# Optimization experiments

Hardware: AMD Instinct MI355X
Metric: run time of the kernel (lower is better)

Reference implementation:

```python
import jax, jax.numpy as jnp
import numpy as np

C, K, DIL = 128, 3, 1
PAD = DIL
KK = K * K
EPS = 1e-5


def setup_inputs() -> dict:
    key = jax.random.key(0)
    k0, k1, k2 = jax.random.split(key, 3)
    B, H, W = 8, 128, 128
    x = jax.random.normal(k0, (B, C, H, W), jnp.float32)
    # small offset-conv weights so predicted offsets are realistic (sub-pixel scale)
    w_off = jax.random.normal(k1, (2 * KK, C, K, K), jnp.float32) * 0.01
    b_off = jnp.zeros((2 * KK,), jnp.float32)
    w_dw = jax.random.normal(k2, (C, 1, K, K), jnp.float32) * (1.0 / 3.0)
    gamma = jnp.ones((C,), jnp.float32)
    beta = jnp.zeros((C,), jnp.float32)
    return {"x": x, "w_off": w_off, "b_off": b_off, "w_dw": w_dw,
            "gamma": gamma, "beta": beta}


def _deform_depthwise(x, offset, w_dw):
    """torchvision-style deform_conv2d, groups=C (depthwise), stride=1."""
    B, C_, H, W = x.shape
    off = offset.reshape(B, KK, 2, H, W)  # (y,x) pairs per kernel tap
    hs = jnp.arange(H, dtype=x.dtype)[None, None, :, None]
    ws = jnp.arange(W, dtype=x.dtype)[None, None, None, :]
    ki = jnp.arange(K, dtype=x.dtype)
    ky = jnp.repeat(ki, K)  # [KK] row index of tap
    kx = jnp.tile(ki, K)    # [KK] col index of tap
    # sampling positions: base grid + dilated tap offset - pad + learned offset
    py = hs + (DIL * ky - PAD)[None, :, None, None] + off[:, :, 0]  # [B,KK,H,W]
    px = ws + (DIL * kx - PAD)[None, :, None, None] + off[:, :, 1]
    y0 = jnp.floor(py)
    x0 = jnp.floor(px)
    ty = py - y0
    tx = px - x0
    y0i = y0.astype(jnp.int32)
    x0i = x0.astype(jnp.int32)

    def gather(xb, yi, xi):
        # zero outside the image (torchvision zero-pad semantics)
        valid = (yi >= 0) & (yi < H) & (xi >= 0) & (xi < W)
        yc = jnp.clip(yi, 0, H - 1)
        xc = jnp.clip(xi, 0, W - 1)
        v = xb[:, yc, xc]  # [C,KK,H,W]
        return v * valid[None].astype(xb.dtype)

    def sample_one(xb, y0b, x0b, tyb, txb):
        v00 = gather(xb, y0b, x0b)
        v01 = gather(xb, y0b, x0b + 1)
        v10 = gather(xb, y0b + 1, x0b)
        v11 = gather(xb, y0b + 1, x0b + 1)
        w00 = (1 - tyb) * (1 - txb)
        w01 = (1 - tyb) * txb
        w10 = tyb * (1 - txb)
        w11 = tyb * txb
        return (v00 * w00[None] + v01 * w01[None]
                + v10 * w10[None] + v11 * w11[None])  # [C,KK,H,W]

    val = jax.vmap(sample_one)(x, y0i, x0i, ty, tx)  # [B,C,KK,H,W]
    # depthwise contraction over the KK taps
    return jnp.einsum('bckhw,ck->bchw', val, w_dw.reshape(C, KK))


def reference(x, w_off, b_off, w_dw, gamma, beta):
    identity = x
    offset = jax.lax.conv_general_dilated(
        x, w_off, window_strides=(1, 1), padding=[(PAD, PAD), (PAD, PAD)],
        dimension_numbers=('NCHW', 'OIHW', 'NCHW'))
    offset = offset + b_off[None, :, None, None]
    out = _deform_depthwise(x, offset, w_dw)
    # BatchNorm2d in training mode (batch statistics), then SiLU
    mean = jnp.mean(out, axis=(0, 2, 3), keepdims=True)
    var = jnp.mean((out - mean) ** 2, axis=(0, 2, 3), keepdims=True)
    out = (out - mean) * jax.lax.rsqrt(var + EPS)
    out = out * gamma[None, :, None, None] + beta[None, :, None, None]
    out = out * jax.nn.sigmoid(out)  # SiLU
    return out + identity
```

## Files before the change

kernel.cpp:

```cpp
#include <hip/hip_runtime.h>
#include <hip/hip_fp16.h>
#include <math.h>

#define Cc 128
#define Hh 128
#define Ww 128
#define Bb 8
#define HW 16384
#define NPIX 131072
#define NOFF 18

typedef unsigned int u32;
typedef _Float16 half8 __attribute__((ext_vector_type(8)));
typedef __attribute__((ext_vector_type(16))) float f32x16;

static __device__ __forceinline__ u32 pack2h(float a, float b){
  __half2 h = __floats2half2_rn(a, b);
  return *(u32*)&h;
}

__global__ __launch_bounds__(256) void k_repack(const float* __restrict__ w_off, const float* __restrict__ w_dw,
                                                u32* __restrict__ wBf, u32* __restrict__ wdt_h){
  int i = blockIdx.x*256 + threadIdx.x;
  if (i < 72*64*4){
    int step = i >> 8;
    int r    = i & 255;
    int lane = r >> 2;
    int q    = r & 3;
    int tap  = step / 8, chunk = step % 8;
    int o    = lane & 31, half = lane >> 5;
    int c0   = chunk*16 + half*8 + 2*q;
    float v0 = (o < NOFF) ? w_off[(size_t)(o*Cc + c0    )*9 + tap] : 0.f;
    float v1 = (o < NOFF) ? w_off[(size_t)(o*Cc + c0 + 1)*9 + tap] : 0.f;
    wBf[i] = pack2h(v0, v1);
  }
  int j = i - 72*64*4;
  if (j >= 0 && j < 9*64){
    int cp = j & 63; int k = j >> 6;
    wdt_h[j] = pack2h(w_dw[(2*cp)*9 + k], w_dw[(2*cp+1)*9 + k]);
  }
}

__global__ __launch_bounds__(256) void k_tx(const float* __restrict__ x, u32* __restrict__ xt16){
  __shared__ float t[128][65];
  int tid = threadIdx.x;
  int b   = blockIdx.x >> 8;
  int hw0 = (blockIdx.x & 255) << 6;
  int lane = tid & 63, wg = tid >> 6;
  const float* xb = x + (size_t)b*Cc*HW;
  #pragma unroll
  for (int k=0;k<32;k++){
    int c = wg + k*4;
    t[c][lane] = xb[(size_t)c*HW + hw0 + lane];
  }
  __syncthreads();
  u32* ob = xt16 + ((size_t)b*HW + hw0)*64;
  int cpair = tid & 63, grp = tid >> 6;
  #pragma unroll
  for (int k=0;k<16;k++){
    int hwl = grp + k*4;
    ob[(size_t)hwl*64 + cpair] = pack2h(t[cpair*2][hwl], t[cpair*2+1][hwl]);
  }
}

__global__ __launch_bounds__(256) void k_offset_mfma(const u32* __restrict__ xt, const u32* __restrict__ wBf,
                                                     const float* __restrict__ b_off, u32* __restrict__ recs){
  __shared__ u32 xl[132][65];
  int tid = threadIdx.x, lane = tid & 63, wv = tid >> 6;
  int b = blockIdx.x >> 7, h = blockIdx.x & 127;
  int row = lane & 31, half = lane >> 5;
  int w = wv*32 + row;

  const u32* xb = xt + (size_t)b*HW*64;
  const uint4* wb = (const uint4*)wBf;

  f32x16 accE, accO;
  #pragma unroll
  for (int i=0;i<16;i++){ accE[i]=0.f; accO[i]=0.f; }

  const u32* xl0 = &xl[0][0];

  #pragma unroll 1
  for (int r=0; r<3; r++){
    int hh = h + r - 1;
    int hc = min(max(hh,0),Hh-1);
    __syncthreads();
    for (int i=tid; i<132*16; i+=256){
      int q = i & 15, p = i >> 4;
      int gc = min(max(p-2, 0), Ww-1);
      *(uint4*)&xl[p][q*4] = *(const uint4*)(xb + ((size_t)(hc*Ww + gc))*64 + q*4);
    }
    __syncthreads();
    bool rowv = (hh>=0)&&(hh<Hh);
    #pragma unroll
    for (int dx=0; dx<3; dx++){
      int t = r*3 + dx;
      int wt = w + dx - 1;
      bool v = rowv && (wt>=0)&&(wt<Ww);
      int base = (w + dx + 1)*65 + half*4;
      #pragma unroll
      for (int ch=0; ch<8; ch++){
        uint4 a = *(const uint4*)(xl0 + base + ch*8);
        if (!v){ a.x=0u; a.y=0u; a.z=0u; a.w=0u; }
        uint4 bf = wb[(t*8+ch)*64 + lane];
        if (ch & 1) accO = __builtin_amdgcn_mfma_f32_32x32x16_f16(*(half8*)&a, *(half8*)&bf, accO, 0, 0, 0);
        else        accE = __builtin_amdgcn_mfma_f32_32x32x16_f16(*(half8*)&a, *(half8*)&bf, accE, 0, 0, 0);
      }
    }
  }
  f32x16 acc = accE + accO;

  __syncthreads();
  float* pivf = (float*)&xl[0][0];
  int o = lane & 31;
  #pragma unroll
  for (int r=0;r<16;r++){
    int pxl = wv*32 + ((r&3) + 8*(r>>2) + 4*half);
    if (o < NOFF) pivf[pxl*21 + o] = acc[r];
  }
  __syncthreads();

  if (tid < 128){
    int wpx = tid;
    float v[NOFF];
    #pragma unroll
    for (int oo=0;oo<NOFF;oo++) v[oo] = pivf[tid*21 + oo] + b_off[oo];

    u32 rec[36];
    #pragma unroll
    for (int kk=0;kk<9;kk++){
      float py = (float)(h + kk/3 - 1) + v[2*kk];
      float qx = (float)(wpx + kk%3 - 1) + v[2*kk+1];
      float fy = floorf(py), fx = floorf(qx);
      float ty = py - fy, tx = qx - fx;
      int y0 = (int)fy, x0 = (int)fx;
      int y1 = y0+1, x1 = x0+1;
      bool vy0 = (y0>=0)&&(y0<Hh), vy1=(y1>=0)&&(y1<Hh);
      bool vx0 = (x0>=0)&&(x0<Ww), vx1=(x1>=0)&&(x1<Ww);
      u32 yc0 = (u32)(min(max(y0,0),Hh-1)*Ww), yc1 = (u32)(min(max(y1,0),Hh-1)*Ww);
      u32 xc0 = (u32)min(max(x0,0),Ww-1),      xc1 = (u32)min(max(x1,0),Ww-1);
      rec[2*kk]   = (yc0+xc0) | ((yc0+xc1)<<16);
      rec[2*kk+1] = (yc1+xc0) | ((yc1+xc1)<<16);
      float c00 = (vy0&&vx0) ? (1.f-ty)*(1.f-tx) : 0.f;
      float c01 = (vy0&&vx1) ? (1.f-ty)*tx       : 0.f;
      float c10 = (vy1&&vx0) ? ty*(1.f-tx)       : 0.f;
      float c11 = (vy1&&vx1) ? ty*tx             : 0.f;
      rec[18+2*kk] = pack2h(c00, c01);
      rec[19+2*kk] = pack2h(c10, c11);
    }
    int pxg = b*HW + h*Ww + wpx;
    uint4* dst = (uint4*)(recs + (size_t)pxg*36);
    #pragma unroll
    for (int q=0;q<9;q++) dst[q] = *(uint4*)(rec + q*4);
  }
}

template<bool F16OUT>
__global__ __launch_bounds__(256) void k_deform_rec(const u32* __restrict__ xt, const u32* __restrict__ recs,
                                                    const u32* __restrict__ wdt_h, float* __restrict__ out,
                                                    u32* __restrict__ dwb, float* __restrict__ bps){
  __shared__ float pivot[16][132];
  int tid = threadIdx.x, lane = tid & 63, wid = tid >> 6;
  int pxb = blockIdx.x * 16;
  int bu = pxb >> 14, hw0 = pxb & 16383;
  int l2 = lane*2;

  __half2 wk2[9];
  #pragma unroll
  for (int k=0;k<9;k++){
    u32 wv = wdt_h[k*64 + lane];
    wk2[k] = *(__half2*)&wv;
  }

  const u32* xbu = xt + (size_t)bu*HW*64;

  #pragma unroll
  for (int i=0;i<4;i++){
    int pu = __builtin_amdgcn_readfirstlane(pxb + wid*4 + i);
    const u32* rec = recs + (size_t)pu*36;

    u32 q[9][4];
    #pragma unroll
    for (int kk=0;kk<9;kk++){
      u32 dA = rec[2*kk], dB = rec[2*kk+1];
      q[kk][0] = xbu[(size_t)(dA & 0xFFFFu)*64 + lane];
      q[kk][1] = xbu[(size_t)(dA >> 16)   *64 + lane];
      q[kk][2] = xbu[(size_t)(dB & 0xFFFFu)*64 + lane];
      q[kk][3] = xbu[(size_t)(dB >> 16)   *64 + lane];
    }

    __half2 acc2 = __floats2half2_rn(0.f, 0.f);
    #pragma unroll
    for (int kk=0;kk<9;kk++){
      u32 uA = rec[18+2*kk], uB = rec[19+2*kk];
      __half2 hA = *(__half2*)&uA, hB = *(__half2*)&uB;
      __half2 q0 = *(__half2*)&q[kk][0], q1 = *(__half2*)&q[kk][1];
      __half2 q2 = *(__half2*)&q[kk][2], q3 = *(__half2*)&q[kk][3];
      __half2 s = __hmul2(__low2half2(hA), q0);
      s = __hfma2(__high2half2(hA), q1, s);
      s = __hfma2(__low2half2(hB),  q2, s);
      s = __hfma2(__high2half2(hB), q3, s);
      acc2 = __hfma2(wk2[kk], s, acc2);
    }
    pivot[wid*4+i][l2]   = __low2float(acc2);
    pivot[wid*4+i][l2+1] = __high2float(acc2);
  }
  __syncthreads();
  #pragma unroll
  for (int it=0; it<2; it++){
    int c = (tid>>2) + it*64, qd = tid & 3;
    float4 r = make_float4(pivot[qd*4+0][c], pivot[qd*4+1][c], pivot[qd*4+2][c], pivot[qd*4+3][c]);
    float s  = (r.x + r.y) + (r.z + r.w);
    float s2 = fmaf(r.x,r.x, fmaf(r.y,r.y, fmaf(r.z,r.z, r.w*r.w)));
    s  += __shfl_down(s, 2, 4);  s  += __shfl_down(s, 1, 4);
    s2 += __shfl_down(s2, 2, 4); s2 += __shfl_down(s2, 1, 4);
    if (qd == 0){
      bps[(size_t)blockIdx.x*256 + c]       = s;
      bps[(size_t)blockIdx.x*256 + 128 + c] = s2;
    }
    if (F16OUT){
      uint2 pp; pp.x = pack2h(r.x, r.y); pp.y = pack2h(r.z, r.w);
      *(uint2*)&dwb[(((size_t)bu*Cc + c)*HW + hw0)/2 + qd*2] = pp;
    } else {
      *(float4*)(out + ((size_t)bu*Cc + c)*HW + hw0 + qd*4) = r;
    }
  }
}

__global__ __launch_bounds__(256) void k_statsr1(const float* __restrict__ bps, float* __restrict__ part2){
  int tid = threadIdx.x;
  size_t base = (size_t)blockIdx.x * 64;
  float a = 0.f;
  for (int r=0;r<64;r++) a += bps[(base + r)*256 + tid];
  part2[blockIdx.x*256 + tid] = a;
}

__global__ __launch_bounds__(256) void k_statsr2(const float* __restrict__ part2, float* __restrict__ mr){
  __shared__ float t[256];
  int tid = threadIdx.x;
  float a = 0.f;
  for (int r=0;r<128;r++) a += part2[r*256 + tid];
  t[tid] = a;
  __syncthreads();
  if (tid < 128){
    float S = t[tid], S2 = t[128 + tid];
    const float invN = 1.f/(float)(Bb*HW);
    float m = S*invN;
    float var = S2*invN - m*m;
    mr[tid]       = m;
    mr[Cc + tid]  = rsqrtf(var + 1e-5f);
  }
}

__global__ __launch_bounds__(256) void k_apply_f32(float* __restrict__ out, const float* __restrict__ x,
                                                   const float* __restrict__ mr, const float* __restrict__ gamma,
                                                   const float* __restrict__ beta){
  int i = blockIdx.x*256 + threadIdx.x;
  int c = (i >> 12) & 127;
  float4 v  = ((const float4*)out)[i];
  float4 xi = ((const float4*)x)[i];
  float m = mr[c], r = mr[Cc+c], g = gamma[c], be = beta[c];
  float* vp = (float*)&v; const float* xp = (const float*)&xi;
  float4 o; float* op = (float*)&o;
  #pragma unroll
  for (int j=0;j<4;j++){
    float t = (vp[j]-m)*r*g + be;
    t = t / (1.f + expf(-t));
    op[j] = t + xp[j];
  }
  ((float4*)out)[i] = o;
}

__global__ __launch_bounds__(256) void k_apply_f16(const u32* __restrict__ dwb, float* __restrict__ out,
                                                   const float* __restrict__ x, const float* __restrict__ mr,
                                                   const float* __restrict__ gamma, const float* __restrict__ beta){
  int i = blockIdx.x*256 + threadIdx.x;
  int c = (i >> 12) & 127;
  uint2 dw = ((const uint2*)dwb)[i];
  float4 xi = ((const float4*)x)[i];
  float m = mr[c], r = mr[Cc+c], g = gamma[c], be = beta[c];
  __half2 d0 = *(__half2*)&dw.x, d1 = *(__half2*)&dw.y;
  float v[4];
  v[0] = __low2float(d0); v[1] = __high2float(d0);
  v[2] = __low2float(d1); v[3] = __high2float(d1);
  const float* xp = (const float*)&xi;
  float4 o; float* op = (float*)&o;
  #pragma unroll
  for (int j=0;j<4;j++){
    float t = (v[j]-m)*r*g + be;
    t = t / (1.f + expf(-t));
    op[j] = t + xp[j];
  }
  ((float4*)out)[i] = o;
}

extern "C" void kernel_launch(void* const* d_in, const int* in_sizes, int n_in,
                              void* d_out, int out_size, void* d_ws, size_t ws_size,
                              hipStream_t stream) {
  const float* x     = (const float*)d_in[0];
  const float* w_off = (const float*)d_in[1];
  const float* b_off = (const float*)d_in[2];
  const float* w_dw  = (const float*)d_in[3];
  const float* gamma = (const float*)d_in[4];
  const float* beta  = (const float*)d_in[5];
  float* out = (float*)d_out;

  u32*   wBf  = (u32*)d_ws;
  u32*   wdt_h= (u32*)d_ws + 23040;
  float* mr   = (float*)d_ws + 24576;
  u32*   recs = (u32*)d_ws + 32768;
  u32*   xt16 = recs + (size_t)NPIX*36;
  float* bps  = (float*)(xt16 + (size_t)NPIX*64);
  float* part2= bps + (size_t)8192*256;
  u32*   dwb  = (u32*)(part2 + 128*256);

  const size_t NEED_B = ((size_t)32768 + (size_t)NPIX*36 + (size_t)NPIX*64
                         + (size_t)8192*256 + 128*256 + (size_t)NPIX*64) * 4;
  bool big = (ws_size >= NEED_B);

  hipLaunchKernelGGL(k_repack, dim3((72*64*4 + 9*64 + 255)/256), dim3(256), 0, stream, w_off, w_dw, wBf, wdt_h);
  hipLaunchKernelGGL(k_tx,     dim3(2048), dim3(256), 0, stream, x, xt16);
  hipLaunchKernelGGL(k_offset_mfma, dim3(1024), dim3(256), 0, stream, xt16, wBf, b_off, recs);

  if (big){
    hipLaunchKernelGGL((k_deform_rec<true>), dim3(NPIX/16), dim3(256), 0, stream, xt16, recs, wdt_h, out, dwb, bps);
  } else {
    hipLaunchKernelGGL((k_deform_rec<false>), dim3(NPIX/16), dim3(256), 0, stream, xt16, recs, wdt_h, out, dwb, bps);
  }
  hipLaunchKernelGGL(k_statsr1, dim3(128), dim3(256), 0, stream, bps, part2);
  hipLaunchKernelGGL(k_statsr2, dim3(1),   dim3(256), 0, stream, part2, mr);
  if (big){
    hipLaunchKernelGGL(k_apply_f16, dim3(NPIX*Cc/4/256), dim3(256), 0, stream, dwb, out, x, mr, gamma, beta);
  } else {
    hipLaunchKernelGGL(k_apply_f32, dim3(NPIX*Cc/4/256), dim3(256), 0, stream, out, x, mr, gamma, beta);
  }
}
```

Baseline: 156.2 us.

## Split offset conv blocks across half-rows and channel halves with LDS reduction

The offset MFMA kernel now covers half a row (64 pixels) per block instead of a full row, and splits the channel reduction across wave pairs. Each pair of waves accumulates half of the K dimension, and the two partial results are summed through shared memory before record generation. The grid doubles to 2048 blocks and shared memory per block shrinks. This aims to raise parallelism and occupancy in the offset stage, at the cost of an extra LDS reduction pass and more halo reloads.

```diff
diff --git a/kernel.cpp b/kernel.cpp
--- a/kernel.cpp
+++ b/kernel.cpp
@@ -65,29 +65,35 @@
 
 __global__ __launch_bounds__(256) void k_offset_mfma(const u32* __restrict__ xt, const u32* __restrict__ wBf,
                                                      const float* __restrict__ b_off, u32* __restrict__ recs){
-  __shared__ u32 xl[132][65];
+  __shared__ u32 xl[68][65];
+  __shared__ float pivf[64][21];
   int tid = threadIdx.x, lane = tid & 63, wv = tid >> 6;
-  int b = blockIdx.x >> 7, h = blockIdx.x & 127;
+  int mw = wv & 1, kh = wv >> 1;
+  int b  = blockIdx.x >> 8;
+  int rm = blockIdx.x & 255;
+  int h  = rm >> 1, wh = rm & 1;
   int row = lane & 31, half = lane >> 5;
-  int w = wv*32 + row;
+  int l = mw*32 + row;
+  int w = wh*64 + l;
 
   const u32* xb = xt + (size_t)b*HW*64;
   const uint4* wb = (const uint4*)wBf;
+  const u32* xl0 = &xl[0][0];
 
   f32x16 accE, accO;
   #pragma unroll
   for (int i=0;i<16;i++){ accE[i]=0.f; accO[i]=0.f; }
 
-  const u32* xl0 = &xl[0][0];
+  int w0c = wh*64 - 2;
 
   #pragma unroll 1
   for (int r=0; r<3; r++){
     int hh = h + r - 1;
     int hc = min(max(hh,0),Hh-1);
     __syncthreads();
-    for (int i=tid; i<132*16; i+=256){
+    for (int i=tid; i<68*16; i+=256){
       int q = i & 15, p = i >> 4;
-      int gc = min(max(p-2, 0), Ww-1);
+      int gc = min(max(w0c + p, 0), Ww-1);
       *(uint4*)&xl[p][q*4] = *(const uint4*)(xb + ((size_t)(hc*Ww + gc))*64 + q*4);
     }
     __syncthreads();
@@ -97,12 +103,12 @@
       int t = r*3 + dx;
       int wt = w + dx - 1;
       bool v = rowv && (wt>=0)&&(wt<Ww);
-      int base = (w + dx + 1)*65 + half*4;
+      int base = (l + dx + 1)*65 + half*4;
       #pragma unroll
-      for (int ch=0; ch<8; ch++){
-        uint4 a = *(const uint4*)(xl0 + base + ch*8);
+      for (int ch=0; ch<4; ch++){
+        uint4 a = *(const uint4*)(xl0 + base + (kh*4+ch)*8);
         if (!v){ a.x=0u; a.y=0u; a.z=0u; a.w=0u; }
-        uint4 bf = wb[(t*8+ch)*64 + lane];
+        uint4 bf = wb[(t*8 + kh*4 + ch)*64 + lane];
         if (ch & 1) accO = __builtin_amdgcn_mfma_f32_32x32x16_f16(*(half8*)&a, *(half8*)&bf, accO, 0, 0, 0);
         else        accE = __builtin_amdgcn_mfma_f32_32x32x16_f16(*(half8*)&a, *(half8*)&bf, accE, 0, 0, 0);
       }
@@ -110,21 +116,30 @@
   }
   f32x16 acc = accE + accO;
 
-  __syncthreads();
-  float* pivf = (float*)&xl[0][0];
   int o = lane & 31;
-  #pragma unroll
-  for (int r=0;r<16;r++){
-    int pxl = wv*32 + ((r&3) + 8*(r>>2) + 4*half);
-    if (o < NOFF) pivf[pxl*21 + o] = acc[r];
-  }
-  __syncthreads();
-
-  if (tid < 128){
-    int wpx = tid;
+  __syncthreads();
+  if (kh == 0){
+    #pragma unroll
+    for (int r=0;r<16;r++){
+      int pxl = mw*32 + ((r&3) + 8*(r>>2) + 4*half);
+      if (o < NOFF) pivf[pxl][o] = acc[r];
+    }
+  }
+  __syncthreads();
+  if (kh == 1){
+    #pragma unroll
+    for (int r=0;r<16;r++){
+      int pxl = mw*32 + ((r&3) + 8*(r>>2) + 4*half);
+      if (o < NOFF) pivf[pxl][o] += acc[r];
+    }
+  }
+  __syncthreads();
+
+  if (tid < 64){
+    int wpx = wh*64 + tid;
     float v[NOFF];
     #pragma unroll
-    for (int oo=0;oo<NOFF;oo++) v[oo] = pivf[tid*21 + oo] + b_off[oo];
+    for (int oo=0;oo<NOFF;oo++) v[oo] = pivf[tid][oo] + b_off[oo];
 
     u32 rec[36];
     #pragma unroll
@@ -320,7 +335,7 @@
 
   hipLaunchKernelGGL(k_repack, dim3((72*64*4 + 9*64 + 255)/256), dim3(256), 0, stream, w_off, w_dw, wBf, wdt_h);
   hipLaunchKernelGGL(k_tx,     dim3(2048), dim3(256), 0, stream, x, xt16);
-  hipLaunchKernelGGL(k_offset_mfma, dim3(1024), dim3(256), 0, stream, xt16, wBf, b_off, recs);
+  hipLaunchKernelGGL(k_offset_mfma, dim3(2048), dim3(256), 0, stream, xt16, wBf, b_off, recs);
 
   if (big){
     hipLaunchKernelGGL((k_deform_rec<true>), dim3(NPIX/16), dim3(256), 0, stream, xt16, recs, wdt_h, out, dwb, bps);
```

New measurement: 158.2 us. Within noise of the previous version (+1.3%).
